# Kernel tuning notes

Hardware: AMD Instinct MI355X
Metric: run time of the kernel (lower is better)

Reference implementation:

```python
import jax, jax.numpy as jnp
import numpy as np

SIGMA = 0.1   # sigma_disc (params[3])
ALPHA = 0.05  # alpha_disc (params[2])


def setup_inputs() -> dict:
    key = jax.random.key(0)
    k1, k2, k3 = jax.random.split(key, 3)
    E, S, T = 3, 8192, 100  # num_events, num_samples, num_bin + num_extra_bin
    logits = jax.random.normal(k1, (E, S, T), dtype=jnp.float32)
    event_out = jax.nn.softmax(logits, axis=-1)  # per-event discrete hazard probs, rows sum to 1
    event_times = jax.random.randint(k2, (S, E), 0, 99).astype(jnp.int32)
    labs = jax.random.randint(k3, (S, E), 0, 2).astype(jnp.int32)
    return {"event_out": event_out, "event_times": event_times, "labs": labs,
            "num_bin": 96, "num_extra_bin": 4}


def _c_loss(event_out, event_times, labs, T):
    # cum[e, k, t] = sum(event_out[e, k, :t+1]); risk with cutoff c = 1 - cum[..., c-1]
    cum = jnp.cumsum(event_out, axis=-1)  # (E, S, T)
    E = event_out.shape[0]
    penalty = jnp.float32(0.0)
    for i in range(E):  # small fixed number of events
        c = cum[i]                    # (S, T)
        t = event_times[:, i]         # (S,)
        lab = labs[:, i]              # (S,)
        had = lab == 1
        # ---- forward concordance (had_event branch) ----
        e_f = jnp.minimum(t + 1, T - 1)              # per-reference-sample cutoff, >= 1
        # risk_f[j, k] = 1 - sum(event_out[k, :e_f[j]]) = 1 - cum[k, e_f[j]-1]
        risk_f = 1.0 - c[:, e_f - 1].T               # (S_j, S_k)
        diff_f = risk_f - jnp.diagonal(risk_f)[:, None]  # comp_risk - reference_risk
        # f_compare: t_k > e_j - 1  OR  (t_k == e_j - 1 AND lab_k == 0)
        mask_f = had[:, None] & ((t[None, :] >= e_f[:, None]) |
                                 ((t[None, :] == e_f[:, None] - 1) & (lab[None, :] == 0)))
        penalty = penalty + jnp.sum(jnp.where(mask_f & (diff_f < 0),
                                              jnp.exp(-diff_f / SIGMA), 0.0))
        # ---- backward concordance (back_c branch, active when t_j > 0) ----
        e_b = jnp.minimum(jnp.where(had, t, t + 1), T - 1)
        risk_b = 1.0 - c[:, jnp.maximum(e_b, 1) - 1].T
        diff_b = risk_b - jnp.diagonal(risk_b)[:, None]
        # b_compare: t_k <= e_j - 1 AND lab_k == 1
        mask_b = (t > 0)[:, None] & (t[None, :] <= e_b[:, None] - 1) & (lab[None, :] == 1)
        penalty = penalty + jnp.sum(jnp.where(mask_b & (diff_b > 0),
                                              jnp.exp(diff_b / SIGMA), 0.0))
    return ALPHA * penalty


def reference(event_out, event_times, labs, num_bin, num_extra_bin):
    return _c_loss(event_out, event_times, labs, num_bin + num_extra_bin)
```

## Files before the change

kernel.cpp:

```cpp
#include <hip/hip_runtime.h>

#define E_CONST 3
#define T_CONST 100
#define C10 10.0f
#define ALPHA_C 0.05f
#define SPLIT 4

__device__ inline int waveInclScan(int v, int lane) {
    #pragma unroll
    for (int off = 1; off < 64; off <<= 1) {
        int n = __shfl_up(v, off, 64);
        if (lane >= off) v += n;
    }
    return v;
}

__global__ __launch_bounds__(512) void combo_kernel(
    const float* __restrict__ event_out, const int* __restrict__ et,
    const int* __restrict__ labs, float* __restrict__ cumT,
    int* __restrict__ perm, int* __restrict__ binStartA,
    int prepBlocks, int S)
{
    __shared__ float tile[64][101];
    __shared__ int histK[2 * T_CONST];
    __shared__ int cursK[2 * T_CONST];
    __shared__ int wsK[8];

    const int tid = threadIdx.x;

    if ((int)blockIdx.x < prepBlocks) {
        const int rowbase = (int)blockIdx.x * 64;
        const float4* __restrict__ src =
            reinterpret_cast<const float4*>(event_out) + (size_t)rowbase * 25;
        for (int idx = tid; idx < 64 * 25; idx += 512) {
            const float4 v = src[idx];
            const int r = idx / 25;
            const int c = idx - r * 25;
            float* d = &tile[r][c * 4];
            d[0] = v.x; d[1] = v.y; d[2] = v.z; d[3] = v.w;
        }
        __syncthreads();
        if (tid < 64) {
            float run = 0.f;
            #pragma unroll 4
            for (int c = 0; c < T_CONST; ++c) { run += tile[tid][c]; tile[tid][c] = run; }
        }
        __syncthreads();
        const int i  = rowbase / S;
        const int s0 = rowbase - i * S;
        float* __restrict__ dst = cumT + (size_t)i * T_CONST * S + s0;
        for (int idx = tid; idx < 64 * T_CONST; idx += 512) {
            const int t = idx >> 6;
            const int r = idx & 63;
            dst[(size_t)t * S + r] = tile[r][t];
        }
        return;
    }

    const int i = (int)blockIdx.x - prepBlocks;
    const int lane = tid & 63, wid = tid >> 6;

    for (int b = tid; b < 2 * T_CONST; b += 512) histK[b] = 0;
    __syncthreads();

    for (int s0 = tid; s0 < S; s0 += 2048) {
        const int sB = s0 + 512, sC = s0 + 1024, sD = s0 + 1536;
        const int tA = et[s0 * E_CONST + i];
        const int lA = labs[s0 * E_CONST + i];
        int tB = 0, lB = 0, tC = 0, lC = 0, tD = 0, lD = 0;
        if (sB < S) { tB = et[sB * E_CONST + i]; lB = labs[sB * E_CONST + i]; }
        if (sC < S) { tC = et[sC * E_CONST + i]; lC = labs[sC * E_CONST + i]; }
        if (sD < S) { tD = et[sD * E_CONST + i]; lD = labs[sD * E_CONST + i]; }
        atomicAdd(&histK[tA * 2 + (1 - lA)], 1);
        if (sB < S) atomicAdd(&histK[tB * 2 + (1 - lB)], 1);
        if (sC < S) atomicAdd(&histK[tC * 2 + (1 - lC)], 1);
        if (sD < S) atomicAdd(&histK[tD * 2 + (1 - lD)], 1);
    }
    __syncthreads();

    const int vK = (tid < 2 * T_CONST) ? histK[tid] : 0;
    int inclK = waveInclScan(vK, lane);
    if (lane == 63) wsK[wid] = inclK;
    __syncthreads();
    int offK = 0;
    for (int w = 0; w < wid; ++w) offK += wsK[w];
    inclK += offK;
    const int exclK = inclK - vK;

    if (tid < 2 * T_CONST) {
        cursK[tid] = exclK;
        binStartA[i * 2 * T_CONST + tid] = exclK;
    }
    __syncthreads();

    for (int s0 = tid; s0 < S; s0 += 2048) {
        const int sB = s0 + 512, sC = s0 + 1024, sD = s0 + 1536;
        const int tA = et[s0 * E_CONST + i];
        const int lA = labs[s0 * E_CONST + i];
        int tB = 0, lB = 0, tC = 0, lC = 0, tD = 0, lD = 0;
        if (sB < S) { tB = et[sB * E_CONST + i]; lB = labs[sB * E_CONST + i]; }
        if (sC < S) { tC = et[sC * E_CONST + i]; lC = labs[sC * E_CONST + i]; }
        if (sD < S) { tD = et[sD * E_CONST + i]; lD = labs[sD * E_CONST + i]; }

        int slot = atomicAdd(&cursK[tA * 2 + (1 - lA)], 1);
        perm[i * S + slot] = s0;
        if (sB < S) { slot = atomicAdd(&cursK[tB * 2 + (1 - lB)], 1); perm[i * S + slot] = sB; }
        if (sC < S) { slot = atomicAdd(&cursK[tC * 2 + (1 - lC)], 1); perm[i * S + slot] = sC; }
        if (sD < S) { slot = atomicAdd(&cursK[tD * 2 + (1 - lD)], 1); perm[i * S + slot] = sD; }
    }
}

__global__ __launch_bounds__(256) void grouppair_kernel(
    const float* __restrict__ cumT, const int* __restrict__ perm,
    const int* __restrict__ et, const int* __restrict__ labs,
    const int* __restrict__ binStartA, float* __restrict__ partials, int S)
{
    __shared__ __align__(16) float elds[2048];
    __shared__ float wsum[4];
    __shared__ int wcnt[4];
    __shared__ int nTot;
    const int tid = threadIdx.x;
    const int lane = tid & 63, wid = tid >> 6;

    int x = (int)blockIdx.x;
    const int sp = x & (SPLIT - 1); x >>= 2;
    const int dir = x & 1;          x >>= 1;
    const int tt = x % T_CONST;
    const int i  = x / T_CONST;

    const int* __restrict__ bs = binStartA + i * 2 * T_CONST;
    int kbeg = 0, kend = 0, colIdx = 0, tref = 0;
    bool active = true;
    if (dir == 0) {
        kbeg = bs[2 * tt]; kend = bs[2 * tt + 1]; colIdx = tt; tref = tt;
    } else {
        const int cb = (T_CONST - 2) - tt;
        if (cb < 0) active = false;
        else { kbeg = (cb == 0) ? bs[2] : bs[2 * cb + 1]; kend = bs[2 * cb + 3];
               colIdx = cb; tref = cb; }
    }
    const int K = kend - kbeg;
    if (K <= 0) active = false;

    float blocktot = 0.f;
    if (active) {
        const int chunk = S / SPLIT;
        const int cbeg = sp * chunk;
        const float* __restrict__ col = cumT + ((size_t)i * T_CONST + colIdx) * S;
        const float sgn = (dir == 0) ? C10 : -C10;

        float ev[8];
        int mask = 0, m = 0;
        #pragma unroll
        for (int j = 0; j < 8; ++j) {
            const int s = cbeg + tid + j * 256;
            const int ts = et[s * E_CONST + i];
            const int ls = labs[s * E_CONST + i];
            const bool mem = (dir == 0)
                ? ((ts > tref) | ((ts == tref) & (ls == 0)))
                : ((ts <= tref) & (ls == 1));
            ev[j] = __expf(sgn * col[s]);
            if (mem) { mask |= (1 << j); ++m; }
        }
        const int incl = waveInclScan(m, lane);
        if (lane == 63) wcnt[wid] = incl;
        __syncthreads();
        int off = 0;
        for (int w = 0; w < wid; ++w) off += wcnt[w];
        int base = incl - m + off;
        #pragma unroll
        for (int j = 0; j < 8; ++j)
            if (mask & (1 << j)) elds[base++] = ev[j];
        if (tid == 255) {
            const int n = base;
            nTot = n;
            const int np = (n + 3) & ~3;
            for (int p = n; p < np; ++p) elds[p] = 0.f;
        }
        __syncthreads();

        const int n = nTot;
        if (n > 0) {
            const int qn4 = ((n + 3) & ~3) >> 2;
            const int kq = tid & 31;
            const int ep = tid >> 5;
            const float4* __restrict__ e4 = reinterpret_cast<const float4*>(elds);
            const int permBase = i * S;
            const int nkc = (K + 31) >> 5;

            for (int kc = 0; kc < nkc; ++kc) {
                const int j = kbeg + (kc << 5) + kq;
                float thr = 1e30f, factor = 0.f;
                if (j < kend) {
                    const float tval = __expf(C10 * col[perm[permBase + j]]);
                    if (dir == 0) { thr = tval;        factor = 1.0f / tval; }
                    else          { thr = 1.0f / tval; factor = tval; }
                }
                float acc = 0.f;
                for (int q = ep; q < qn4; q += 8) {
                    const float4 v = e4[q];
                    acc += (v.x > thr) ? v.x : 0.f;
                    acc += (v.y > thr) ? v.y : 0.f;
                    acc += (v.z > thr) ? v.z : 0.f;
                    acc += (v.w > thr) ? v.w : 0.f;
                }
                blocktot += acc * factor;
            }
        }
    }

    for (int off = 32; off > 0; off >>= 1) blocktot += __shfl_down(blocktot, off, 64);
    if (lane == 0) wsum[wid] = blocktot;
    __syncthreads();
    if (tid == 0) partials[blockIdx.x] = wsum[0] + wsum[1] + wsum[2] + wsum[3];
}

__global__ __launch_bounds__(1024) void reduce_kernel(
    const float* __restrict__ partials, int n, float* __restrict__ out)
{
    const int tid = threadIdx.x;
    float s0 = 0.f, s1 = 0.f, s2 = 0.f, s3 = 0.f;
    const int n4 = n & ~3;
    for (int idx = tid * 4; idx < n4; idx += 4096) {
        const float4 v = *reinterpret_cast<const float4*>(partials + idx);
        s0 += v.x; s1 += v.y; s2 += v.z; s3 += v.w;
    }
    for (int idx = n4 + tid; idx < n; idx += 1024) s0 += partials[idx];
    float sum = (s0 + s1) + (s2 + s3);
    for (int off = 32; off > 0; off >>= 1) sum += __shfl_down(sum, off, 64);
    __shared__ float wsum[16];
    const int lane = tid & 63, wd = tid >> 6;
    if (lane == 0) wsum[wd] = sum;
    __syncthreads();
    if (tid == 0) {
        float t = 0.f;
        for (int w = 0; w < 16; ++w) t += wsum[w];
        out[0] = ALPHA_C * t;
    }
}

__global__ __launch_bounds__(64) void prep_fb_kernel(
    const float* __restrict__ event_out, const int* __restrict__ et,
    const int* __restrict__ labs, float* __restrict__ cumT,
    int* __restrict__ tlA, int S)
{
    const int gid = blockIdx.x * 64 + threadIdx.x;
    const int i = gid / S;
    const int s = gid - i * S;
    const float4* __restrict__ row =
        reinterpret_cast<const float4*>(event_out + (size_t)gid * T_CONST);
    float* __restrict__ base = cumT + (size_t)i * T_CONST * S + s;
    float run = 0.f;
    #pragma unroll
    for (int c = 0; c < T_CONST / 4; ++c) {
        const float4 v = row[c];
        const float c0 = run + v.x;
        const float c1 = c0 + v.y;
        const float c2 = c1 + v.z;
        const float c3 = c2 + v.w;
        base[(size_t)(4 * c + 0) * S] = c0;
        base[(size_t)(4 * c + 1) * S] = c1;
        base[(size_t)(4 * c + 2) * S] = c2;
        base[(size_t)(4 * c + 3) * S] = c3;
        run = c3;
    }
    const int t   = et[s * E_CONST + i];
    const int lab = labs[s * E_CONST + i];
    tlA[i * S + s] = (t & 0xffff) | (lab << 16);
}

__global__ __launch_bounds__(256) void pair_fb_kernel(
    const float* __restrict__ cumT, const int* __restrict__ tlA,
    float* __restrict__ partials, int S)
{
    const int bx = blockIdx.x;
    const int i = bx / S;
    const int k = bx - i * S;
    const int base = i * S;
    const int tlk = tlA[base + k];
    const int t_k = tlk & 0xffff;
    const int lab_k = tlk >> 16;
    const bool doF = (lab_k == 1);
    const bool doB = (t_k > 0);
    float sum = 0.f;
    if (doF || doB) {
        const int cb = lab_k ? (t_k > 0 ? t_k - 1 : 0) : t_k;
        const float* __restrict__ colF = cumT + ((size_t)i * T_CONST + t_k) * S;
        const float* __restrict__ colB = cumT + ((size_t)i * T_CONST + cb)  * S;
        const float vf_k = colF[k];
        const float vb_k = colB[k];
        const int* __restrict__ tlp = tlA + base;
        for (int s = threadIdx.x; s < S; s += 256) {
            const int tls = tlp[s];
            const int t_s = tls & 0xffff;
            const int lab_s = tls >> 16;
            if (doF) {
                const float vs = colF[s];
                const bool c = (t_s > t_k) | ((t_s == t_k) & (lab_s == 0));
                if (c & (vs > vf_k)) sum += __expf((vs - vf_k) * C10);
            }
            if (doB) {
                const float vs = colB[s];
                const bool c = (t_s <= cb) & (lab_s == 1);
                if (c & (vb_k > vs)) sum += __expf((vb_k - vs) * C10);
            }
        }
    }
    for (int off = 32; off > 0; off >>= 1) sum += __shfl_down(sum, off, 64);
    __shared__ float wsum[4];
    const int lane = threadIdx.x & 63, wd = threadIdx.x >> 6;
    if (lane == 0) wsum[wd] = sum;
    __syncthreads();
    if (threadIdx.x == 0) partials[bx] = wsum[0] + wsum[1] + wsum[2] + wsum[3];
}

extern "C" void kernel_launch(void* const* d_in, const int* in_sizes, int n_in,
                              void* d_out, int out_size, void* d_ws, size_t ws_size,
                              hipStream_t stream)
{
    const float* event_out = (const float*)d_in[0];
    const int*   et        = (const int*)d_in[1];
    const int*   labsp     = (const int*)d_in[2];
    const int S = in_sizes[1] / E_CONST;

    const size_t colElems = (size_t)E_CONST * T_CONST * S;
    const size_t esElems  = (size_t)E_CONST * S;
    const int    gpBlocks = E_CONST * T_CONST * 2 * SPLIT;

    char* p = (char*)d_ws;
    float* cumT     = (float*)p; p += colElems * 4;
    int*   perm     = (int*)p;   p += esElems * 4;
    int*   binStart = (int*)p;   p += (size_t)E_CONST * 2 * T_CONST * 4;
    float* partials = (float*)p; p += (size_t)gpBlocks * 4;
    const size_t needed = (size_t)(p - (char*)d_ws);
    const size_t fallback_needed = colElems * 4 + esElems * 4 * 2;

    const int prepBlocks = (E_CONST * S) / 64;

    if (ws_size >= needed && (E_CONST * S) % 64 == 0 && (S / SPLIT) == 2048) {
        hipLaunchKernelGGL(combo_kernel, dim3(prepBlocks + E_CONST), dim3(512), 0, stream,
                           event_out, et, labsp, cumT, perm, binStart,
                           prepBlocks, S);
        hipLaunchKernelGGL(grouppair_kernel, dim3(gpBlocks), dim3(256), 0, stream,
                           cumT, perm, et, labsp, binStart, partials, S);
        hipLaunchKernelGGL(reduce_kernel, dim3(1), dim3(1024), 0, stream,
                           partials, gpBlocks, (float*)d_out);
    } else if (ws_size >= fallback_needed) {
        const int nB = E_CONST * S;
        float* cumT2     = (float*)d_ws;
        int*   tlA2      = (int*)(cumT2 + colElems);
        float* partials2 = (float*)(tlA2 + esElems);
        hipLaunchKernelGGL(prep_fb_kernel, dim3(E_CONST * S / 64), dim3(64), 0, stream,
                           event_out, et, labsp, cumT2, tlA2, S);
        hipLaunchKernelGGL(pair_fb_kernel, dim3(nB), dim3(256), 0, stream,
                           cumT2, tlA2, partials2, S);
        hipLaunchKernelGGL(reduce_kernel, dim3(1), dim3(1024), 0, stream,
                           partials2, nB, (float*)d_out);
    }
}
```

Measured before the change: 107.1 us.

## Replace global perm/bin sort with in-block compaction of threshold samples

Removes the histogram and counting-sort pass that built a per-event permutation and bin starts. Each grouppair block now scans all S samples itself in 256-sample chunks, compacts the matching reference samples' exp values into shared memory, and runs the pairwise comparison on each batch of up to 2048. This drops the serialized 3-block sort stage from the first kernel. In exchange every one of the 2400 blocks rereads et/labs for all S samples and adds many extra syncthreads per chunk.

```diff
diff --git a/kernel.cpp b/kernel.cpp
--- a/kernel.cpp
+++ b/kernel.cpp
@@ -15,107 +15,44 @@
     return v;
 }
 
-__global__ __launch_bounds__(512) void combo_kernel(
-    const float* __restrict__ event_out, const int* __restrict__ et,
-    const int* __restrict__ labs, float* __restrict__ cumT,
-    int* __restrict__ perm, int* __restrict__ binStartA,
-    int prepBlocks, int S)
+__global__ __launch_bounds__(512) void prep_kernel(
+    const float* __restrict__ event_out, float* __restrict__ cumT, int S)
 {
     __shared__ float tile[64][101];
-    __shared__ int histK[2 * T_CONST];
-    __shared__ int cursK[2 * T_CONST];
-    __shared__ int wsK[8];
-
     const int tid = threadIdx.x;
-
-    if ((int)blockIdx.x < prepBlocks) {
-        const int rowbase = (int)blockIdx.x * 64;
-        const float4* __restrict__ src =
-            reinterpret_cast<const float4*>(event_out) + (size_t)rowbase * 25;
-        for (int idx = tid; idx < 64 * 25; idx += 512) {
-            const float4 v = src[idx];
-            const int r = idx / 25;
-            const int c = idx - r * 25;
-            float* d = &tile[r][c * 4];
-            d[0] = v.x; d[1] = v.y; d[2] = v.z; d[3] = v.w;
-        }
-        __syncthreads();
-        if (tid < 64) {
-            float run = 0.f;
-            #pragma unroll 4
-            for (int c = 0; c < T_CONST; ++c) { run += tile[tid][c]; tile[tid][c] = run; }
-        }
-        __syncthreads();
-        const int i  = rowbase / S;
-        const int s0 = rowbase - i * S;
-        float* __restrict__ dst = cumT + (size_t)i * T_CONST * S + s0;
-        for (int idx = tid; idx < 64 * T_CONST; idx += 512) {
-            const int t = idx >> 6;
-            const int r = idx & 63;
-            dst[(size_t)t * S + r] = tile[r][t];
-        }
-        return;
-    }
-
-    const int i = (int)blockIdx.x - prepBlocks;
-    const int lane = tid & 63, wid = tid >> 6;
-
-    for (int b = tid; b < 2 * T_CONST; b += 512) histK[b] = 0;
-    __syncthreads();
-
-    for (int s0 = tid; s0 < S; s0 += 2048) {
-        const int sB = s0 + 512, sC = s0 + 1024, sD = s0 + 1536;
-        const int tA = et[s0 * E_CONST + i];
-        const int lA = labs[s0 * E_CONST + i];
-        int tB = 0, lB = 0, tC = 0, lC = 0, tD = 0, lD = 0;
-        if (sB < S) { tB = et[sB * E_CONST + i]; lB = labs[sB * E_CONST + i]; }
-        if (sC < S) { tC = et[sC * E_CONST + i]; lC = labs[sC * E_CONST + i]; }
-        if (sD < S) { tD = et[sD * E_CONST + i]; lD = labs[sD * E_CONST + i]; }
-        atomicAdd(&histK[tA * 2 + (1 - lA)], 1);
-        if (sB < S) atomicAdd(&histK[tB * 2 + (1 - lB)], 1);
-        if (sC < S) atomicAdd(&histK[tC * 2 + (1 - lC)], 1);
-        if (sD < S) atomicAdd(&histK[tD * 2 + (1 - lD)], 1);
-    }
-    __syncthreads();
-
-    const int vK = (tid < 2 * T_CONST) ? histK[tid] : 0;
-    int inclK = waveInclScan(vK, lane);
-    if (lane == 63) wsK[wid] = inclK;
-    __syncthreads();
-    int offK = 0;
-    for (int w = 0; w < wid; ++w) offK += wsK[w];
-    inclK += offK;
-    const int exclK = inclK - vK;
-
-    if (tid < 2 * T_CONST) {
-        cursK[tid] = exclK;
-        binStartA[i * 2 * T_CONST + tid] = exclK;
-    }
-    __syncthreads();
-
-    for (int s0 = tid; s0 < S; s0 += 2048) {
-        const int sB = s0 + 512, sC = s0 + 1024, sD = s0 + 1536;
-        const int tA = et[s0 * E_CONST + i];
-        const int lA = labs[s0 * E_CONST + i];
-        int tB = 0, lB = 0, tC = 0, lC = 0, tD = 0, lD = 0;
-        if (sB < S) { tB = et[sB * E_CONST + i]; lB = labs[sB * E_CONST + i]; }
-        if (sC < S) { tC = et[sC * E_CONST + i]; lC = labs[sC * E_CONST + i]; }
-        if (sD < S) { tD = et[sD * E_CONST + i]; lD = labs[sD * E_CONST + i]; }
-
-        int slot = atomicAdd(&cursK[tA * 2 + (1 - lA)], 1);
-        perm[i * S + slot] = s0;
-        if (sB < S) { slot = atomicAdd(&cursK[tB * 2 + (1 - lB)], 1); perm[i * S + slot] = sB; }
-        if (sC < S) { slot = atomicAdd(&cursK[tC * 2 + (1 - lC)], 1); perm[i * S + slot] = sC; }
-        if (sD < S) { slot = atomicAdd(&cursK[tD * 2 + (1 - lD)], 1); perm[i * S + slot] = sD; }
+    const int rowbase = (int)blockIdx.x * 64;
+    const float4* __restrict__ src =
+        reinterpret_cast<const float4*>(event_out) + (size_t)rowbase * 25;
+    for (int idx = tid; idx < 64 * 25; idx += 512) {
+        const float4 v = src[idx];
+        const int r = idx / 25;
+        const int c = idx - r * 25;
+        float* d = &tile[r][c * 4];
+        d[0] = v.x; d[1] = v.y; d[2] = v.z; d[3] = v.w;
+    }
+    __syncthreads();
+    if (tid < 64) {
+        float run = 0.f;
+        #pragma unroll 4
+        for (int c = 0; c < T_CONST; ++c) { run += tile[tid][c]; tile[tid][c] = run; }
+    }
+    __syncthreads();
+    const int i  = rowbase / S;
+    const int s0 = rowbase - i * S;
+    float* __restrict__ dst = cumT + (size_t)i * T_CONST * S + s0;
+    for (int idx = tid; idx < 64 * T_CONST; idx += 512) {
+        const int t = idx >> 6;
+        const int r = idx & 63;
+        dst[(size_t)t * S + r] = tile[r][t];
     }
 }
 
 __global__ __launch_bounds__(256) void grouppair_kernel(
-    const float* __restrict__ cumT, const int* __restrict__ perm,
-    const int* __restrict__ et, const int* __restrict__ labs,
-    const int* __restrict__ binStartA, float* __restrict__ partials, int S)
+    const float* __restrict__ cumT, const int* __restrict__ et,
+    const int* __restrict__ labs, float* __restrict__ partials, int S)
 {
     __shared__ __align__(16) float elds[2048];
+    __shared__ float tlds[2048];
     __shared__ float wsum[4];
     __shared__ int wcnt[4];
     __shared__ int nTot;
@@ -128,26 +65,21 @@
     const int tt = x % T_CONST;
     const int i  = x / T_CONST;
 
-    const int* __restrict__ bs = binStartA + i * 2 * T_CONST;
-    int kbeg = 0, kend = 0, colIdx = 0, tref = 0;
+    int colIdx = 0, tref = 0;
     bool active = true;
-    if (dir == 0) {
-        kbeg = bs[2 * tt]; kend = bs[2 * tt + 1]; colIdx = tt; tref = tt;
-    } else {
+    if (dir == 0) { colIdx = tt; tref = tt; }
+    else {
         const int cb = (T_CONST - 2) - tt;
         if (cb < 0) active = false;
-        else { kbeg = (cb == 0) ? bs[2] : bs[2 * cb + 1]; kend = bs[2 * cb + 3];
-               colIdx = cb; tref = cb; }
-    }
-    const int K = kend - kbeg;
-    if (K <= 0) active = false;
+        else { colIdx = cb; tref = cb; }
+    }
 
     float blocktot = 0.f;
     if (active) {
+        const float* __restrict__ col = cumT + ((size_t)i * T_CONST + colIdx) * S;
+        const float sgn = (dir == 0) ? C10 : -C10;
         const int chunk = S / SPLIT;
         const int cbeg = sp * chunk;
-        const float* __restrict__ col = cumT + ((size_t)i * T_CONST + colIdx) * S;
-        const float sgn = (dir == 0) ? C10 : -C10;
 
         float ev[8];
         int mask = 0, m = 0;
@@ -162,22 +94,23 @@
             ev[j] = __expf(sgn * col[s]);
             if (mem) { mask |= (1 << j); ++m; }
         }
-        const int incl = waveInclScan(m, lane);
-        if (lane == 63) wcnt[wid] = incl;
-        __syncthreads();
-        int off = 0;
-        for (int w = 0; w < wid; ++w) off += wcnt[w];
-        int base = incl - m + off;
-        #pragma unroll
-        for (int j = 0; j < 8; ++j)
-            if (mask & (1 << j)) elds[base++] = ev[j];
-        if (tid == 255) {
-            const int n = base;
-            nTot = n;
-            const int np = (n + 3) & ~3;
-            for (int p = n; p < np; ++p) elds[p] = 0.f;
+        {
+            const int incl = waveInclScan(m, lane);
+            if (lane == 63) wcnt[wid] = incl;
+            __syncthreads();
+            int off = 0;
+            for (int w = 0; w < wid; ++w) off += wcnt[w];
+            int base = incl - m + off;
+            #pragma unroll
+            for (int j = 0; j < 8; ++j)
+                if (mask & (1 << j)) elds[base++] = ev[j];
+            if (tid == 255) {
+                nTot = base;
+                const int np = (base + 3) & ~3;
+                for (int p = base; p < np; ++p) elds[p] = 0.f;
+            }
+            __syncthreads();
         }
-        __syncthreads();
 
         const int n = nTot;
         if (n > 0) {
@@ -185,26 +118,50 @@
             const int kq = tid & 31;
             const int ep = tid >> 5;
             const float4* __restrict__ e4 = reinterpret_cast<const float4*>(elds);
-            const int permBase = i * S;
-            const int nkc = (K + 31) >> 5;
-
-            for (int kc = 0; kc < nkc; ++kc) {
-                const int j = kbeg + (kc << 5) + kq;
-                float thr = 1e30f, factor = 0.f;
-                if (j < kend) {
-                    const float tval = __expf(C10 * col[perm[permBase + j]]);
-                    if (dir == 0) { thr = tval;        factor = 1.0f / tval; }
-                    else          { thr = 1.0f / tval; factor = tval; }
+            const int nChunks = S >> 8;
+
+            int cChunk = 0;
+            while (cChunk < nChunks) {
+                int Kb = 0;
+                while (cChunk < nChunks && Kb + 256 <= 2048) {
+                    const int s = (cChunk << 8) + tid;
+                    const int ts = et[s * E_CONST + i];
+                    const int ls = labs[s * E_CONST + i];
+                    bool isThr;
+                    if (dir == 0) isThr = (ts == tref) & (ls == 1);
+                    else          isThr = ((ts == tref + 1) & (ls == 1)) |
+                                          ((tref > 0) & (ts == tref) & (ls == 0));
+                    const int tm = isThr ? 1 : 0;
+                    const int tincl = waveInclScan(tm, lane);
+                    if (lane == 63) wcnt[wid] = tincl;
+                    __syncthreads();
+                    int toff = Kb;
+                    for (int w = 0; w < wid; ++w) toff += wcnt[w];
+                    if (isThr) tlds[toff + tincl - tm] = __expf(C10 * col[s]);
+                    Kb += wcnt[0] + wcnt[1] + wcnt[2] + wcnt[3];
+                    ++cChunk;
+                    __syncthreads();
                 }
-                float acc = 0.f;
-                for (int q = ep; q < qn4; q += 8) {
-                    const float4 v = e4[q];
-                    acc += (v.x > thr) ? v.x : 0.f;
-                    acc += (v.y > thr) ? v.y : 0.f;
-                    acc += (v.z > thr) ? v.z : 0.f;
-                    acc += (v.w > thr) ? v.w : 0.f;
+                const int nkc = (Kb + 31) >> 5;
+                for (int kc = 0; kc < nkc; ++kc) {
+                    const int j = (kc << 5) + kq;
+                    float thr = 1e30f, factor = 0.f;
+                    if (j < Kb) {
+                        const float tval = tlds[j];
+                        if (dir == 0) { thr = tval;        factor = 1.0f / tval; }
+                        else          { thr = 1.0f / tval; factor = tval; }
+                    }
+                    float acc = 0.f;
+                    for (int q = ep; q < qn4; q += 8) {
+                        const float4 v = e4[q];
+                        acc += (v.x > thr) ? v.x : 0.f;
+                        acc += (v.y > thr) ? v.y : 0.f;
+                        acc += (v.z > thr) ? v.z : 0.f;
+                        acc += (v.w > thr) ? v.w : 0.f;
+                    }
+                    blocktot += acc * factor;
                 }
-                blocktot += acc * factor;
+                __syncthreads();
             }
         }
     }
@@ -329,20 +286,18 @@
 
     char* p = (char*)d_ws;
     float* cumT     = (float*)p; p += colElems * 4;
-    int*   perm     = (int*)p;   p += esElems * 4;
-    int*   binStart = (int*)p;   p += (size_t)E_CONST * 2 * T_CONST * 4;
     float* partials = (float*)p; p += (size_t)gpBlocks * 4;
     const size_t needed = (size_t)(p - (char*)d_ws);
     const size_t fallback_needed = colElems * 4 + esElems * 4 * 2;
 
     const int prepBlocks = (E_CONST * S) / 64;
 
-    if (ws_size >= needed && (E_CONST * S) % 64 == 0 && (S / SPLIT) == 2048) {
-        hipLaunchKernelGGL(combo_kernel, dim3(prepBlocks + E_CONST), dim3(512), 0, stream,
-                           event_out, et, labsp, cumT, perm, binStart,
-                           prepBlocks, S);
+    if (ws_size >= needed && (E_CONST * S) % 64 == 0 &&
+        (S / SPLIT) == 2048 && (S % 256) == 0) {
+        hipLaunchKernelGGL(prep_kernel, dim3(prepBlocks), dim3(512), 0, stream,
+                           event_out, cumT, S);
         hipLaunchKernelGGL(grouppair_kernel, dim3(gpBlocks), dim3(256), 0, stream,
-                           cumT, perm, et, labsp, binStart, partials, S);
+                           cumT, et, labsp, partials, S);
         hipLaunchKernelGGL(reduce_kernel, dim3(1), dim3(1024), 0, stream,
                            partials, gpBlocks, (float*)d_out);
     } else if (ws_size >= fallback_needed) {
```

Result: slower. 150.7 us (+40.7%).
